# Kernel tuning notes

Hardware: AMD Instinct MI355X
Metric: run time of the kernel (lower is better)

The kernel has to match this reference:

```python
import jax, jax.numpy as jnp
import numpy as np


def _grid_mesh(n):
    ys, xs = np.meshgrid(np.arange(n), np.arange(n), indexing='ij')
    verts = np.stack([xs, ys, np.zeros_like(xs)], -1).reshape(-1, 3).astype(np.float32) / (n - 1)
    idx = np.arange(n * n).reshape(n, n)
    v00 = idx[:-1, :-1].ravel(); v01 = idx[:-1, 1:].ravel()
    v10 = idx[1:, :-1].ravel(); v11 = idx[1:, 1:].ravel()
    faces = np.concatenate([np.stack([v00, v10, v01], 1), np.stack([v01, v10, v11], 1)], 0).astype(np.int32)
    e = np.concatenate([faces[:, [0, 1]], faces[:, [1, 2]], faces[:, [2, 0]]], 0)
    e = np.unique(np.sort(e, axis=1), axis=0).astype(np.int32)
    return verts, faces, e


def setup_inputs() -> dict:
    N_GRID, B, S = 200, 2, 5000
    verts_np, faces_np, edges_np = _grid_mesh(N_GRID)
    verts_np[:, 2] = 0.1 * np.sin(2 * np.pi * verts_np[:, 0]) * np.sin(2 * np.pi * verts_np[:, 1])
    key = jax.random.key(0)
    k1, k2, k3, k4 = jax.random.split(key, 4)
    verts_std = jnp.asarray(verts_np)
    verts_scr = verts_std[None] + 5e-4 * jax.random.normal(k1, (B,) + verts_std.shape, jnp.float32)
    xy = jax.random.uniform(k2, (B, S, 2), jnp.float32)
    z = 0.1 * jnp.sin(2 * jnp.pi * xy[..., 0]) * jnp.sin(2 * jnp.pi * xy[..., 1])
    trg_points = jnp.concatenate([xy, z[..., None]], -1)
    rand_face_u = jax.random.uniform(k3, (B, S), jnp.float32)
    rand_bary = jax.random.uniform(k4, (B, S, 2), jnp.float32)
    return {
        'verts_scr': verts_scr,
        'verts_std': verts_std,
        'trg_points': trg_points,
        'rand_face_u': rand_face_u,
        'rand_bary': rand_bary,
        'faces': jnp.asarray(faces_np),
        'edges': jnp.asarray(edges_np),
    }


def _cot_edges(verts, faces):
    # pytorch3d cot_laplacian: per-face cotangents, symmetrized edge list (6F entries).
    v0, v1, v2 = verts[faces[:, 0]], verts[faces[:, 1]], verts[faces[:, 2]]
    A = jnp.linalg.norm(v1 - v2, axis=1)
    B = jnp.linalg.norm(v0 - v2, axis=1)
    C = jnp.linalg.norm(v0 - v1, axis=1)
    A2, B2, C2 = A * A, B * B, C * C
    s = 0.5 * (A + B + C)
    area = jnp.sqrt(jnp.clip(s * (s - A) * (s - B) * (s - C), 1e-12, None))
    cot = jnp.stack([B2 + C2 - A2, A2 + C2 - B2, A2 + B2 - C2], axis=1) / (4.0 * area[:, None])
    ii = faces[:, jnp.array([1, 2, 0])].reshape(-1)
    jj = faces[:, jnp.array([2, 0, 1])].reshape(-1)
    src = jnp.concatenate([ii, jj])
    dst = jnp.concatenate([jj, ii])
    w = jnp.concatenate([cot.reshape(-1), cot.reshape(-1)])
    return src, dst, w


def _sample_points(verts, faces, u_face, r_bary):
    # area-weighted face sampling + pytorch3d barycentric coords
    v0, v1, v2 = verts[faces[:, 0]], verts[faces[:, 1]], verts[faces[:, 2]]
    areas = 0.5 * jnp.linalg.norm(jnp.cross(v1 - v0, v2 - v0), axis=1)
    cdf = jnp.cumsum(areas) / jnp.sum(areas)
    fidx = jnp.clip(jnp.searchsorted(cdf, u_face), 0, faces.shape[0] - 1)
    su = jnp.sqrt(r_bary[:, 0])
    w0, w1, w2 = 1.0 - su, su * (1.0 - r_bary[:, 1]), su * r_bary[:, 1]
    return w0[:, None] * v0[fidx] + w1[:, None] * v1[fidx] + w2[:, None] * v2[fidx]


def _chamfer(x, y):
    # squared-distance chamfer, mean over points then batch (pytorch3d defaults)
    d = (jnp.sum(x * x, -1)[:, :, None] + jnp.sum(y * y, -1)[:, None, :]
         - 2.0 * jnp.einsum('bsd,btd->bst', x, y))
    return jnp.min(d, 2).mean() + jnp.min(d, 1).mean()


def _forward(verts_scr, verts_std, trg_points, rand_face_u, rand_bary, faces, edges):
    Vn = verts_std.shape[0]
    # chamfer between sampled src surface points and target point cloud
    sample_scr = jax.vmap(lambda v, u, r: _sample_points(v, faces, u, r))(verts_scr, rand_face_u, rand_bary)
    loss_p0 = _chamfer(sample_scr, trg_points)
    loss_n1 = jnp.asarray(1e-5, verts_scr.dtype)  # tensor-target branch

    # cot laplacian smoothing (method='cot')
    def lap_one(v):
        src, dst, w = _cot_edges(v, faces)
        Lv = jax.ops.segment_sum(w[:, None] * v[dst], src, num_segments=Vn)
        rw = jax.ops.segment_sum(w, src, num_segments=Vn)
        inv = jnp.where(rw > 0, 1.0 / jnp.maximum(rw, 1e-12), 0.0)
        return jnp.linalg.norm(Lv * inv[:, None] - v, axis=1).mean()

    loss_lap = jax.vmap(lap_one)(verts_scr).mean()

    # edge loss against mean edge length of the std mesh
    target_len = jnp.linalg.norm(verts_std[edges[:, 0]] - verts_std[edges[:, 1]], axis=1).mean()
    elen = jnp.linalg.norm(verts_scr[:, edges[:, 0]] - verts_scr[:, edges[:, 1]], axis=-1)
    loss_edge = ((elen - target_len) ** 2).mean()

    # ARAP rigid loss on std-mesh cot connectivity/weights
    src, dst, w = _cot_edges(verts_std, faces)
    e_std = verts_std[src] - verts_std[dst]

    def rigid_one(v):
        e_scr = v[src] - v[dst]
        S = jax.ops.segment_sum(w[:, None, None] * e_std[:, :, None] * e_scr[:, None, :], src, num_segments=Vn)
        U, _, Vt = jnp.linalg.svd(S)
        R = jnp.matmul(jnp.swapaxes(Vt, -1, -2), jnp.swapaxes(U, -1, -2))
        flip = jnp.where(jnp.linalg.det(R) < 0, -1.0, 1.0)
        Vt2 = Vt.at[:, -1, :].multiply(flip[:, None])
        R = jnp.matmul(jnp.swapaxes(Vt2, -1, -2), jnp.swapaxes(U, -1, -2))
        res = e_scr - jnp.einsum('eij,ej->ei', R[src], e_std)
        return jax.ops.segment_sum(w * jnp.sum(res * res, 1), src, num_segments=Vn)

    loss_rigid = jax.vmap(rigid_one)(verts_scr).mean()
    return jnp.stack([loss_p0, loss_n1, loss_lap, loss_edge, loss_rigid])


def reference(verts_scr, verts_std, trg_points, rand_face_u, rand_bary, faces, edges):
    return _forward(verts_scr, verts_std, trg_points, rand_face_u, rand_bary, faces, edges)
```

## Files before the change

kernel.cpp:

```cpp
#include <hip/hip_runtime.h>
#include <math.h>

#define TPB 256
#define MAXDEG 8

static __device__ __forceinline__ void atomAddD(double* p, double v) {
  __hip_atomic_fetch_add(p, v, __ATOMIC_RELAXED, __HIP_MEMORY_SCOPE_AGENT);
}

static __device__ __forceinline__ double bredsum(double v) {
  __shared__ double sb[TPB];
  int t = threadIdx.x;
  sb[t] = v;
  __syncthreads();
  for (int o = TPB / 2; o > 0; o >>= 1) {
    if (t < o) sb[t] += sb[t + o];
    __syncthreads();
  }
  double r = sb[0];
  __syncthreads();
  return r;
}

template <int p, int q, int r>
static __device__ __forceinline__ void jrot(double A[3][3], double V[3][3]) {
  double apq = A[p][q];
  if (apq == 0.0) return;
  double app = A[p][p], aqq = A[q][q];
  double theta = (aqq - app) / (2.0 * apq);
  double t = 1.0 / (fabs(theta) + sqrt(theta * theta + 1.0));
  if (theta < 0.0) t = -t;
  double c = 1.0 / sqrt(t * t + 1.0), sn = t * c;
  A[p][p] = app - t * apq;
  A[q][q] = aqq + t * apq;
  A[p][q] = 0.0;
  A[q][p] = 0.0;
  double arp = A[r][p], arq = A[r][q];
  A[r][p] = c * arp - sn * arq; A[p][r] = A[r][p];
  A[r][q] = sn * arp + c * arq; A[q][r] = A[r][q];
#pragma unroll
  for (int k = 0; k < 3; k++) {
    double vkp = V[k][p], vkq = V[k][q];
    V[k][p] = c * vkp - sn * vkq;
    V[k][q] = sn * vkp + c * vkq;
  }
}

#define ESWAP(la, lax, lay, laz, lb, lbx, lby, lbz)                       \
  if (la < lb) {                                                          \
    double t_;                                                            \
    t_ = la; la = lb; lb = t_;                                            \
    t_ = lax; lax = lbx; lbx = t_;                                        \
    t_ = lay; lay = lby; lby = t_;                                        \
    t_ = laz; laz = lbz; lbz = t_;                                        \
  }

static __device__ void kabschR(const double S[3][3], double R9[9]) {
  double A[3][3];
#pragma unroll
  for (int a = 0; a < 3; a++)
#pragma unroll
    for (int c = 0; c < 3; c++)
      A[a][c] = S[0][a] * S[0][c] + S[1][a] * S[1][c] + S[2][a] * S[2][c];
  double V[3][3] = {{1, 0, 0}, {0, 1, 0}, {0, 0, 1}};
  for (int sw = 0; sw < 12; sw++) {
    double off = fabs(A[0][1]) + fabs(A[0][2]) + fabs(A[1][2]);
    double dia = fabs(A[0][0]) + fabs(A[1][1]) + fabs(A[2][2]);
    if (!(off > dia * 1e-15)) break;
    jrot<0, 1, 2>(A, V);
    jrot<0, 2, 1>(A, V);
    jrot<1, 2, 0>(A, V);
  }
  double l0 = A[0][0], l1 = A[1][1], l2 = A[2][2];
  double a0x = V[0][0], a0y = V[1][0], a0z = V[2][0];
  double a1x = V[0][1], a1y = V[1][1], a1z = V[2][1];
  double a2x = V[0][2], a2y = V[1][2], a2z = V[2][2];
  ESWAP(l0, a0x, a0y, a0z, l1, a1x, a1y, a1z);
  ESWAP(l0, a0x, a0y, a0z, l2, a2x, a2y, a2z);
  ESWAP(l1, a1x, a1y, a1z, l2, a2x, a2y, a2z);
  double R00 = 1, R01 = 0, R02 = 0, R10 = 0, R11 = 1, R12 = 0, R20 = 0, R21 = 0, R22 = 1;
  double b1x = S[0][0] * a0x + S[0][1] * a0y + S[0][2] * a0z;
  double b1y = S[1][0] * a0x + S[1][1] * a0y + S[1][2] * a0z;
  double b1z = S[2][0] * a0x + S[2][1] * a0y + S[2][2] * a0z;
  double b2x = S[0][0] * a1x + S[0][1] * a1y + S[0][2] * a1z;
  double b2y = S[1][0] * a1x + S[1][1] * a1y + S[1][2] * a1z;
  double b2z = S[2][0] * a1x + S[2][1] * a1y + S[2][2] * a1z;
  double n1 = sqrt(b1x * b1x + b1y * b1y + b1z * b1z);
  if (n1 > 1e-300 && isfinite(n1)) {
    double u1x = b1x / n1, u1y = b1y / n1, u1z = b1z / n1;
    double dp = u1x * b2x + u1y * b2y + u1z * b2z;
    b2x -= dp * u1x; b2y -= dp * u1y; b2z -= dp * u1z;
    double n2 = sqrt(b2x * b2x + b2y * b2y + b2z * b2z);
    double u2x, u2y, u2z;
    if (n2 > n1 * 1e-14) {
      u2x = b2x / n2; u2y = b2y / n2; u2z = b2z / n2;
    } else {
      double f0 = fabs(u1x), f1 = fabs(u1y), f2 = fabs(u1z);
      double e0, e1, e2;
      if (f0 <= f1 && f0 <= f2) { e0 = 1.0 - u1x * u1x; e1 = -u1x * u1y; e2 = -u1x * u1z; }
      else if (f1 <= f2)        { e0 = -u1y * u1x; e1 = 1.0 - u1y * u1y; e2 = -u1y * u1z; }
      else                      { e0 = -u1z * u1x; e1 = -u1z * u1y; e2 = 1.0 - u1z * u1z; }
      double nw = sqrt(e0 * e0 + e1 * e1 + e2 * e2);
      u2x = e0 / nw; u2y = e1 / nw; u2z = e2 / nw;
    }
    double u3x = u1y * u2z - u1z * u2y;
    double u3y = u1z * u2x - u1x * u2z;
    double u3z = u1x * u2y - u1y * u2x;
    double w3x = a0y * a1z - a0z * a1y;
    double w3y = a0z * a1x - a0x * a1z;
    double w3z = a0x * a1y - a0y * a1x;
    R00 = a0x * u1x + a1x * u2x + w3x * u3x;
    R01 = a0x * u1y + a1x * u2y + w3x * u3y;
    R02 = a0x * u1z + a1x * u2z + w3x * u3z;
    R10 = a0y * u1x + a1y * u2x + w3y * u3x;
    R11 = a0y * u1y + a1y * u2y + w3y * u3y;
    R12 = a0y * u1z + a1y * u2z + w3y * u3z;
    R20 = a0z * u1x + a1z * u2x + w3z * u3x;
    R21 = a0z * u1y + a1z * u2y + w3z * u3y;
    R22 = a0z * u1z + a1z * u2z + w3z * u3z;
  }
  R9[0] = R00; R9[1] = R01; R9[2] = R02;
  R9[3] = R10; R9[4] = R11; R9[5] = R12;
  R9[6] = R20; R9[7] = R21; R9[8] = R22;
}

static __device__ __forceinline__ void heronCots(double A2, double B2, double C2,
                                                 double* c0, double* c1, double* c2) {
  double A = sqrt(A2), Bl = sqrt(B2), C = sqrt(C2);
  double s = 0.5 * (A + Bl + C);
  double pr = s * (s - A) * (s - Bl) * (s - C);
  pr = pr < 1e-12 ? 1e-12 : pr;
  double inv4 = 1.0 / (4.0 * sqrt(pr));
  *c0 = (B2 + C2 - A2) * inv4;
  *c1 = (A2 + C2 - B2) * inv4;
  *c2 = (A2 + B2 - C2) * inv4;
}

__global__ void kPrep(const float* vscr, const float* vstd, const int* faces,
                      const int* edges, double* cdf, double* ccot, double* scot,
                      int* adjcnt, int4* adjtab, double* accEdgeStd,
                      int B, int Vn, int F, int E) {
  int i = blockIdx.x * TPB + threadIdx.x;
  if (i < B * F) {
    int b = i / F, f = i % F;
    const float* vb = vscr + (size_t)b * Vn * 3;
    int i0 = faces[f * 3], i1 = faces[f * 3 + 1], i2 = faces[f * 3 + 2];
    {
      double p0x = vb[i0 * 3], p0y = vb[i0 * 3 + 1], p0z = vb[i0 * 3 + 2];
      double p1x = vb[i1 * 3], p1y = vb[i1 * 3 + 1], p1z = vb[i1 * 3 + 2];
      double p2x = vb[i2 * 3], p2y = vb[i2 * 3 + 1], p2z = vb[i2 * 3 + 2];
      double ax = p1x - p0x, ay = p1y - p0y, az = p1z - p0z;
      double bx = p2x - p0x, by = p2y - p0y, bz = p2z - p0z;
      double cx = ay * bz - az * by, cy = az * bx - ax * bz, cz = ax * by - ay * bx;
      cdf[i] = 0.5 * sqrt(cx * cx + cy * cy + cz * cz);
      double dx = p1x - p2x, dy = p1y - p2y, dz = p1z - p2z;
      double A2 = dx * dx + dy * dy + dz * dz;
      double B2 = bx * bx + by * by + bz * bz;
      double C2 = ax * ax + ay * ay + az * az;
      double c0, c1, c2;
      heronCots(A2, B2, C2, &c0, &c1, &c2);
      ccot[(size_t)i * 3 + 0] = c0;
      ccot[(size_t)i * 3 + 1] = c1;
      ccot[(size_t)i * 3 + 2] = c2;
    }
    if (b == 0) {
      double p0x = vstd[i0 * 3], p0y = vstd[i0 * 3 + 1], p0z = vstd[i0 * 3 + 2];
      double p1x = vstd[i1 * 3], p1y = vstd[i1 * 3 + 1], p1z = vstd[i1 * 3 + 2];
      double p2x = vstd[i2 * 3], p2y = vstd[i2 * 3 + 1], p2z = vstd[i2 * 3 + 2];
      double ax = p1x - p0x, ay = p1y - p0y, az = p1z - p0z;
      double bx = p2x - p0x, by = p2y - p0y, bz = p2z - p0z;
      double dx = p1x - p2x, dy = p1y - p2y, dz = p1z - p2z;
      double A2 = dx * dx + dy * dy + dz * dz;
      double B2 = bx * bx + by * by + bz * bz;
      double C2 = ax * ax + ay * ay + az * az;
      double c0, c1, c2;
      heronCots(A2, B2, C2, &c0, &c1, &c2);
      scot[(size_t)f * 3 + 0] = c0;
      scot[(size_t)f * 3 + 1] = c1;
      scot[(size_t)f * 3 + 2] = c2;
      int f3 = f * 3;
      int s0 = atomicAdd(&adjcnt[i0], 1);
      if (s0 < MAXDEG) adjtab[(size_t)i0 * MAXDEG + s0] = make_int4(i1, i2, f3 + 1, f3 + 2);
      int s1 = atomicAdd(&adjcnt[i1], 1);
      if (s1 < MAXDEG) adjtab[(size_t)i1 * MAXDEG + s1] = make_int4(i2, i0, f3 + 2, f3 + 0);
      int s2 = atomicAdd(&adjcnt[i2], 1);
      if (s2 < MAXDEG) adjtab[(size_t)i2 * MAXDEG + s2] = make_int4(i0, i1, f3 + 0, f3 + 1);
    }
  }
  double eval = 0.0;
  if (i < E) {
    int e0 = edges[(size_t)i * 2], e1 = edges[(size_t)i * 2 + 1];
    double dx = (double)vstd[e0 * 3 + 0] - vstd[e1 * 3 + 0];
    double dy = (double)vstd[e0 * 3 + 1] - vstd[e1 * 3 + 1];
    double dz = (double)vstd[e0 * 3 + 2] - vstd[e1 * 3 + 2];
    eval = sqrt(dx * dx + dy * dy + dz * dz);
  }
  double r = bredsum(eval);
  if (threadIdx.x == 0) atomAddD(accEdgeStd, r);
}

__global__ void kScanFused(double* a, double* bsum, double* boffs, int F, int nc,
                           int B, int* cnt) {
  int blk = blockIdx.x;
  int b = blk / nc, c = blk % nc;
  int t = threadIdx.x, lane = t & 63, wid = t >> 6;
  int f = c * 1024 + t;
  size_t idx = (size_t)b * F + f;
  double v = (f < F) ? a[idx] : 0.0;
  double x = v;
#pragma unroll
  for (int o = 1; o < 64; o <<= 1) {
    double y = __shfl_up(x, o, 64);
    if (lane >= o) x += y;
  }
  __shared__ double wsum[16];
  __shared__ double woffs[16];
  if (lane == 63) wsum[wid] = x;
  __syncthreads();
  if (wid == 0) {
    double s = (lane < 16) ? wsum[lane] : 0.0;
    double xs = s;
#pragma unroll
    for (int o = 1; o < 16; o <<= 1) {
      double y = __shfl_up(xs, o, 64);
      if (lane >= o) xs += y;
    }
    double ex = __shfl_up(xs, 1, 64);
    if (lane < 16) woffs[lane] = (lane == 0) ? 0.0 : ex;
  }
  __syncthreads();
  x += woffs[wid];
  if (f < F) a[idx] = x;
  if (t == 1023) bsum[(size_t)b * nc + c] = x;
  __syncthreads();
  __shared__ int amlast;
  if (t == 0) {
    __threadfence();
    int old = __hip_atomic_fetch_add(cnt, 1, __ATOMIC_ACQ_REL, __HIP_MEMORY_SCOPE_AGENT);
    amlast = (old == (int)gridDim.x - 1) ? 1 : 0;
  }
  __syncthreads();
  if (amlast && wid == 0) {
    for (int bb = 0; bb < B; bb++) {
      double carry = 0.0;
      for (int base = 0; base < nc; base += 64) {
        int cc = base + lane;
        double s = (cc < nc) ? bsum[(size_t)bb * nc + cc] : 0.0;
        double xs = s;
#pragma unroll
        for (int o = 1; o < 64; o <<= 1) {
          double y = __shfl_up(xs, o, 64);
          if (lane >= o) xs += y;
        }
        double ex = __shfl_up(xs, 1, 64);
        double excl = (lane == 0) ? 0.0 : ex;
        if (cc < nc) boffs[(size_t)bb * nc + cc] = carry + excl;
        carry += __shfl(xs, 63, 64);
      }
    }
  }
}

__global__ void kSample(const float* verts, const int* faces, const double* cdf,
                        const double* bsum, const double* boffs,
                        const float* rfu, const float* rbary, float* samples,
                        int B, int Vn, int F, int S, int nc) {
  int i = blockIdx.x * blockDim.x + threadIdx.x;
  if (i >= B * S) return;
  int b = i / S;
  const double* bo = boffs + (size_t)b * nc;
  const double* bs = bsum + (size_t)b * nc;
  double total = bo[nc - 1] + bs[nc - 1];
  double tgt = (double)rfu[i] * total;
  int lo = 0, hi = nc;
  while (lo < hi) {
    int m = (lo + hi) >> 1;
    if (bo[m] + bs[m] < tgt) lo = m + 1; else hi = m;
  }
  int c = lo < nc ? lo : nc - 1;
  double thr = tgt - bo[c];
  const double* cc = cdf + (size_t)b * F + (size_t)c * 1024;
  int lim = F - c * 1024; if (lim > 1024) lim = 1024;
  lo = 0; hi = lim;
  while (lo < hi) {
    int m = (lo + hi) >> 1;
    if (cc[m] < thr) lo = m + 1; else hi = m;
  }
  int j = lo < lim ? lo : lim - 1;
  int f = c * 1024 + j;
  const float* vb = verts + (size_t)b * Vn * 3;
  int i0 = faces[f * 3], i1 = faces[f * 3 + 1], i2 = faces[f * 3 + 2];
  float r0 = rbary[(size_t)i * 2], r1 = rbary[(size_t)i * 2 + 1];
  float su = sqrtf(r0);
  float w0 = 1.f - su, w1 = su * (1.f - r1), w2 = su * r1;
  samples[(size_t)i * 3 + 0] = w0 * vb[i0 * 3 + 0] + w1 * vb[i1 * 3 + 0] + w2 * vb[i2 * 3 + 0];
  samples[(size_t)i * 3 + 1] = w0 * vb[i0 * 3 + 1] + w1 * vb[i1 * 3 + 1] + w2 * vb[i2 * 3 + 1];
  samples[(size_t)i * 3 + 2] = w0 * vb[i0 * 3 + 2] + w1 * vb[i1 * 3 + 2] + w2 * vb[i2 * 3 + 2];
}

__global__ void kChamferBoth(const float* smp, const float* trg, unsigned* rowmin,
                             int B, int S) {
  int z = blockIdx.z;
  int dir = z / B, b = z % B;
  const float* X = dir ? trg : smp;
  const float* Y = dir ? smp : trg;
  int i = blockIdx.x * TPB + threadIdx.x;
  int j0 = blockIdx.y * TPB;
  int n = min(TPB, S - j0);
  __shared__ float4 sy[TPB];
  const float* Yb = Y + ((size_t)b * S + j0) * 3;
  if ((int)threadIdx.x < n) {
    int t = threadIdx.x;
    sy[t] = make_float4(Yb[t * 3], Yb[t * 3 + 1], Yb[t * 3 + 2], 0.f);
  }
  __syncthreads();
  if (i >= S) return;
  const float* Xb = X + (size_t)b * S * 3;
  float x0 = Xb[i * 3], x1 = Xb[i * 3 + 1], x2 = Xb[i * 3 + 2];
  float inf = __int_as_float(0x7f800000);
  float m0 = inf, m1 = inf, m2 = inf, m3 = inf;
  int k = 0;
  for (; k + 4 <= n; k += 4) {
    float4 y0 = sy[k], y1 = sy[k + 1], y2 = sy[k + 2], y3 = sy[k + 3];
    float a0 = x0 - y0.x, b0 = x1 - y0.y, c0 = x2 - y0.z;
    float a1 = x0 - y1.x, b1 = x1 - y1.y, c1 = x2 - y1.z;
    float a2 = x0 - y2.x, b2 = x1 - y2.y, c2 = x2 - y2.z;
    float a3 = x0 - y3.x, b3 = x1 - y3.y, c3 = x2 - y3.z;
    m0 = fminf(m0, a0 * a0 + b0 * b0 + c0 * c0);
    m1 = fminf(m1, a1 * a1 + b1 * b1 + c1 * c1);
    m2 = fminf(m2, a2 * a2 + b2 * b2 + c2 * c2);
    m3 = fminf(m3, a3 * a3 + b3 * b3 + c3 * c3);
  }
  for (; k < n; k++) {
    float4 y = sy[k];
    float a = x0 - y.x, bb = x1 - y.y, cc = x2 - y.z;
    m0 = fminf(m0, a * a + bb * bb + cc * cc);
  }
  float mn = fminf(fminf(m0, m1), fminf(m2, m3));
  atomicMin(&rowmin[((size_t)dir * B + b) * S + i], __float_as_uint(mn));
}

__global__ void kMisc(const unsigned* rm, int nrm, const float* vscr, const int* edges,
                      int B, int Vn, int E, const double* tacc,
                      double* accCh, double* accEd) {
  int i = blockIdx.x * TPB + threadIdx.x;
  double v = 0.0;
  if (i < nrm) v = (double)__uint_as_float(rm[i]);
  double r = bredsum(v);
  if (threadIdx.x == 0) atomAddD(accCh, r);
  double tl = tacc[0] / (double)E;
  double val = 0.0;
  if (i < B * E) {
    int b = i / E, e = i % E;
    const float* vb = vscr + (size_t)b * Vn * 3;
    int e0 = edges[(size_t)e * 2], e1 = edges[(size_t)e * 2 + 1];
    double dx = (double)vb[e0 * 3 + 0] - vb[e1 * 3 + 0];
    double dy = (double)vb[e0 * 3 + 1] - vb[e1 * 3 + 1];
    double dz = (double)vb[e0 * 3 + 2] - vb[e1 * 3 + 2];
    double l = sqrt(dx * dx + dy * dy + dz * dz);
    double d = l - tl;
    val = d * d;
  }
  double r2 = bredsum(val);
  if (threadIdx.x == 0) atomAddD(accEd, r2);
}

__global__ void kVertexFin(const float* vstd, const float* vscr,
                           const int* cnt, const int4* adjtab, const double* scot,
                           const double* ccot, int B, int Vn, int F,
                           double* accum, int* done, float* out, int S, int E) {
  int idx = blockIdx.x * TPB + threadIdx.x;
  double vlap = 0.0, vrig = 0.0;
  if (idx < B * Vn) {
    int b = idx / Vn, v = idx % Vn;
    const float* cb = vscr + (size_t)b * Vn * 3;
    const double* ccb = ccot + (size_t)b * F * 3;
    double pasx = vstd[v * 3], pasy = vstd[v * 3 + 1], pasz = vstd[v * 3 + 2];
    double pacx = cb[v * 3], pacy = cb[v * 3 + 1], pacz = cb[v * 3 + 2];
    int n = cnt[v];
    if (n > MAXDEG) n = MAXDEG;
    const int4* at = adjtab + (size_t)v * MAXDEG;
    double S00 = 0, S01 = 0, S02 = 0, S10 = 0, S11 = 0, S12 = 0, S20 = 0, S21 = 0, S22 = 0;
    double Lx = 0, Ly = 0, Lz = 0, rw = 0, Qs = 0, Qc = 0;
    for (int k = 0; k < n; k++) {
      int4 e = at[k];
      int jb = e.x, jc = e.y;
      double cBs = scot[e.z], cCs = scot[e.w];
      double cBc = ccb[e.z], cCc = ccb[e.w];
      double pbsx = vstd[jb * 3], pbsy = vstd[jb * 3 + 1], pbsz = vstd[jb * 3 + 2];
      double pcsx = vstd[jc * 3], pcsy = vstd[jc * 3 + 1], pcsz = vstd[jc * 3 + 2];
      double pbcx = cb[jb * 3], pbcy = cb[jb * 3 + 1], pbcz = cb[jb * 3 + 2];
      double pccx = cb[jc * 3], pccy = cb[jc * 3 + 1], pccz = cb[jc * 3 + 2];
      Lx += cCc * pbcx + cBc * pccx;
      Ly += cCc * pbcy + cBc * pccy;
      Lz += cCc * pbcz + cBc * pccz;
      rw += cBc + cCc;
      double e1sx = pasx - pbsx, e1sy = pasy - pbsy, e1sz = pasz - pbsz;
      double e2sx = pasx - pcsx, e2sy = pasy - pcsy, e2sz = pasz - pcsz;
      double e1cx = pacx - pbcx, e1cy = pacy - pbcy, e1cz = pacz - pbcz;
      double e2cx = pacx - pccx, e2cy = pacy - pccy, e2cz = pacz - pccz;
      S00 += cCs * e1sx * e1cx + cBs * e2sx * e2cx;
      S01 += cCs * e1sx * e1cy + cBs * e2sx * e2cy;
      S02 += cCs * e1sx * e1cz + cBs * e2sx * e2cz;
      S10 += cCs * e1sy * e1cx + cBs * e2sy * e2cx;
      S11 += cCs * e1sy * e1cy + cBs * e2sy * e2cy;
      S12 += cCs * e1sy * e1cz + cBs * e2sy * e2cz;
      S20 += cCs * e1sz * e1cx + cBs * e2sz * e2cx;
      S21 += cCs * e1sz * e1cy + cBs * e2sz * e2cy;
      S22 += cCs * e1sz * e1cz + cBs * e2sz * e2cz;
      Qs += cCs * (e1sx * e1sx + e1sy * e1sy + e1sz * e1sz)
          + cBs * (e2sx * e2sx + e2sy * e2sy + e2sz * e2sz);
      Qc += cCs * (e1cx * e1cx + e1cy * e1cy + e1cz * e1cz)
          + cBs * (e2cx * e2cx + e2cy * e2cy + e2cz * e2cz);
    }
    double inv = (rw > 0.0) ? 1.0 / fmax(rw, 1e-12) : 0.0;
    double dx = Lx * inv - pacx, dy = Ly * inv - pacy, dz = Lz * inv - pacz;
    vlap = sqrt(dx * dx + dy * dy + dz * dz);
    double S[3][3] = {{S00, S01, S02}, {S10, S11, S12}, {S20, S21, S22}};
    double R9[9];
    kabschR(S, R9);
    double trRS = R9[0] * S00 + R9[1] * S10 + R9[2] * S20
                + R9[3] * S01 + R9[4] * S11 + R9[5] * S21
                + R9[6] * S02 + R9[7] * S12 + R9[8] * S22;
    vrig = Qc + Qs - 2.0 * trRS;
  }
  double r1 = bredsum(vlap);
  if (threadIdx.x == 0) atomAddD(accum + 1, r1);
  double r2 = bredsum(vrig);
  if (threadIdx.x == 0) atomAddD(accum + 4, r2);
  __shared__ int amlast;
  if (threadIdx.x == 0) {
    __threadfence();
    int old = __hip_atomic_fetch_add(done, 1, __ATOMIC_ACQ_REL, __HIP_MEMORY_SCOPE_AGENT);
    amlast = (old == (int)gridDim.x - 1) ? 1 : 0;
  }
  __syncthreads();
  if (amlast && threadIdx.x == 0) {
    double a0 = __hip_atomic_load(accum + 0, __ATOMIC_RELAXED, __HIP_MEMORY_SCOPE_AGENT);
    double a1 = __hip_atomic_load(accum + 1, __ATOMIC_RELAXED, __HIP_MEMORY_SCOPE_AGENT);
    double a3 = __hip_atomic_load(accum + 3, __ATOMIC_RELAXED, __HIP_MEMORY_SCOPE_AGENT);
    double a4 = __hip_atomic_load(accum + 4, __ATOMIC_RELAXED, __HIP_MEMORY_SCOPE_AGENT);
    out[0] = (float)(a0 / ((double)B * S));
    out[1] = 1e-5f;
    out[2] = (float)(a1 / ((double)B * Vn));
    out[3] = (float)(a3 / ((double)B * E));
    out[4] = (float)(a4 / ((double)B * Vn));
  }
}

extern "C" void kernel_launch(void* const* d_in, const int* in_sizes, int n_in,
                              void* d_out, int out_size, void* d_ws, size_t ws_size,
                              hipStream_t stream) {
  const float* vscr = (const float*)d_in[0];
  const float* vstd = (const float*)d_in[1];
  const float* trg  = (const float*)d_in[2];
  const float* rfu  = (const float*)d_in[3];
  const float* rby  = (const float*)d_in[4];
  const int* faces  = (const int*)d_in[5];
  const int* edges  = (const int*)d_in[6];
  float* out = (float*)d_out;

  int nVs = in_sizes[1];
  int Vn = nVs / 3;
  int B = in_sizes[0] / nVs;
  int S = in_sizes[3] / B;
  int F = in_sizes[5] / 3;
  int E = in_sizes[6] / 2;
  int nc = (F + 1023) / 1024;

  char* p = (char*)d_ws;
  auto alloc = [&](size_t bytes) -> void* {
    void* r = (void*)p;
    p += (bytes + 255) & ~(size_t)255;
    return r;
  };
  double* cdf   = (double*)alloc((size_t)B * F * sizeof(double));
  double* bsum  = (double*)alloc((size_t)B * nc * sizeof(double));
  double* boffs = (double*)alloc((size_t)B * nc * sizeof(double));
  double* scot  = (double*)alloc((size_t)F * 3 * sizeof(double));
  double* ccot  = (double*)alloc((size_t)B * F * 3 * sizeof(double));
  float* samples   = (float*)alloc((size_t)B * S * 3 * sizeof(float));
  unsigned* rowmin = (unsigned*)alloc((size_t)2 * B * S * sizeof(unsigned));
  int4* adjtab  = (int4*)alloc((size_t)Vn * MAXDEG * sizeof(int4));
  size_t zbytes = (size_t)Vn * sizeof(int) + 8 * sizeof(int) + 8 * sizeof(double);
  char* zbase   = (char*)alloc(zbytes);
  int* adjcnt   = (int*)zbase;
  int* cnts     = (int*)(zbase + (size_t)Vn * sizeof(int));
  double* accum = (double*)(zbase + (size_t)Vn * sizeof(int) + 8 * sizeof(int));

  hipMemsetAsync(zbase, 0, zbytes, stream);
  int nrm = 2 * B * S;
  hipMemsetAsync(rowmin, 0xFF, (size_t)nrm * sizeof(unsigned), stream);

  int BF = B * F;
  kPrep<<<(BF + TPB - 1) / TPB, TPB, 0, stream>>>(vscr, vstd, faces, edges, cdf, ccot,
                                                  scot, adjcnt, adjtab, accum + 2,
                                                  B, Vn, F, E);
  kScanFused<<<B * nc, 1024, 0, stream>>>(cdf, bsum, boffs, F, nc, B, cnts + 0);
  kSample<<<(B * S + TPB - 1) / TPB, TPB, 0, stream>>>(vscr, faces, cdf, bsum, boffs,
                                                       rfu, rby, samples, B, Vn, F, S, nc);
  dim3 cg((S + TPB - 1) / TPB, (S + TPB - 1) / TPB, 2 * B);
  kChamferBoth<<<cg, TPB, 0, stream>>>(samples, trg, rowmin, B, S);
  int nmisc = nrm > B * E ? nrm : B * E;
  kMisc<<<(nmisc + TPB - 1) / TPB, TPB, 0, stream>>>(rowmin, nrm, vscr, edges, B, Vn, E,
                                                     accum + 2, accum + 0, accum + 3);
  kVertexFin<<<(B * Vn + TPB - 1) / TPB, TPB, 0, stream>>>(vstd, vscr, adjcnt, adjtab,
                                                           scot, ccot, B, Vn, F,
                                                           accum, cnts + 1, out, S, E);
}
```

Measured before the change: 197.4 us.

## Fuse vertex ARAP/Laplacian work with chamfer blocks, fold rowmin init into prep

Merges the per-vertex Laplacian/ARAP kernel and the chamfer nearest-neighbour kernel into one launch: the leading blocks handle vertices and the remaining blocks handle chamfer tiles, so the two independent workloads run concurrently. The misc reduction and the final output write are merged into one last kernel. The rowmin memset moves into kPrep, and the Jacobi sweep cap drops from 12 to 8. Together these remove two launches and a memset and let the double-precision vertex work overlap the FP32 chamfer work. The risks are an inactive branch holding registers and shared memory in every block, and slightly less converged eigenvectors.

```diff
diff --git a/kernel.cpp b/kernel.cpp
--- a/kernel.cpp
+++ b/kernel.cpp
@@ -63,7 +63,7 @@
     for (int c = 0; c < 3; c++)
       A[a][c] = S[0][a] * S[0][c] + S[1][a] * S[1][c] + S[2][a] * S[2][c];
   double V[3][3] = {{1, 0, 0}, {0, 1, 0}, {0, 0, 1}};
-  for (int sw = 0; sw < 12; sw++) {
+  for (int sw = 0; sw < 8; sw++) {
     double off = fabs(A[0][1]) + fabs(A[0][2]) + fabs(A[1][2]);
     double dia = fabs(A[0][0]) + fabs(A[1][1]) + fabs(A[2][2]);
     if (!(off > dia * 1e-15)) break;
@@ -139,8 +139,9 @@
 __global__ void kPrep(const float* vscr, const float* vstd, const int* faces,
                       const int* edges, double* cdf, double* ccot, double* scot,
                       int* adjcnt, int4* adjtab, double* accEdgeStd,
-                      int B, int Vn, int F, int E) {
+                      unsigned* rowmin, int nrm, int B, int Vn, int F, int E) {
   int i = blockIdx.x * TPB + threadIdx.x;
+  if (i < nrm) rowmin[i] = 0xFFFFFFFFu;
   if (i < B * F) {
     int b = i / F, f = i % F;
     const float* vb = vscr + (size_t)b * Vn * 3;
@@ -298,57 +299,125 @@
   samples[(size_t)i * 3 + 2] = w0 * vb[i0 * 3 + 2] + w1 * vb[i1 * 3 + 2] + w2 * vb[i2 * 3 + 2];
 }
 
-__global__ void kChamferBoth(const float* smp, const float* trg, unsigned* rowmin,
-                             int B, int S) {
-  int z = blockIdx.z;
-  int dir = z / B, b = z % B;
-  const float* X = dir ? trg : smp;
-  const float* Y = dir ? smp : trg;
-  int i = blockIdx.x * TPB + threadIdx.x;
-  int j0 = blockIdx.y * TPB;
-  int n = min(TPB, S - j0);
-  __shared__ float4 sy[TPB];
-  const float* Yb = Y + ((size_t)b * S + j0) * 3;
-  if ((int)threadIdx.x < n) {
-    int t = threadIdx.x;
-    sy[t] = make_float4(Yb[t * 3], Yb[t * 3 + 1], Yb[t * 3 + 2], 0.f);
-  }
-  __syncthreads();
-  if (i >= S) return;
-  const float* Xb = X + (size_t)b * S * 3;
-  float x0 = Xb[i * 3], x1 = Xb[i * 3 + 1], x2 = Xb[i * 3 + 2];
-  float inf = __int_as_float(0x7f800000);
-  float m0 = inf, m1 = inf, m2 = inf, m3 = inf;
-  int k = 0;
-  for (; k + 4 <= n; k += 4) {
-    float4 y0 = sy[k], y1 = sy[k + 1], y2 = sy[k + 2], y3 = sy[k + 3];
-    float a0 = x0 - y0.x, b0 = x1 - y0.y, c0 = x2 - y0.z;
-    float a1 = x0 - y1.x, b1 = x1 - y1.y, c1 = x2 - y1.z;
-    float a2 = x0 - y2.x, b2 = x1 - y2.y, c2 = x2 - y2.z;
-    float a3 = x0 - y3.x, b3 = x1 - y3.y, c3 = x2 - y3.z;
-    m0 = fminf(m0, a0 * a0 + b0 * b0 + c0 * c0);
-    m1 = fminf(m1, a1 * a1 + b1 * b1 + c1 * c1);
-    m2 = fminf(m2, a2 * a2 + b2 * b2 + c2 * c2);
-    m3 = fminf(m3, a3 * a3 + b3 * b3 + c3 * c3);
-  }
-  for (; k < n; k++) {
-    float4 y = sy[k];
-    float a = x0 - y.x, bb = x1 - y.y, cc = x2 - y.z;
-    m0 = fminf(m0, a * a + bb * bb + cc * cc);
-  }
-  float mn = fminf(fminf(m0, m1), fminf(m2, m3));
-  atomicMin(&rowmin[((size_t)dir * B + b) * S + i], __float_as_uint(mn));
-}
-
-__global__ void kMisc(const unsigned* rm, int nrm, const float* vscr, const int* edges,
-                      int B, int Vn, int E, const double* tacc,
-                      double* accCh, double* accEd) {
+__global__ void kFat(const float* vstd, const float* vscr,
+                     const int* cnt, const int4* adjtab, const double* scot,
+                     const double* ccot, const float* smp, const float* trg,
+                     unsigned* rowmin, int nv, int ncx, int B, int Vn, int F, int S,
+                     double* accum) {
+  if ((int)blockIdx.x < nv) {
+    int idx = blockIdx.x * TPB + threadIdx.x;
+    double vlap = 0.0, vrig = 0.0;
+    if (idx < B * Vn) {
+      int b = idx / Vn, v = idx % Vn;
+      const float* cb = vscr + (size_t)b * Vn * 3;
+      const double* ccb = ccot + (size_t)b * F * 3;
+      double pasx = vstd[v * 3], pasy = vstd[v * 3 + 1], pasz = vstd[v * 3 + 2];
+      double pacx = cb[v * 3], pacy = cb[v * 3 + 1], pacz = cb[v * 3 + 2];
+      int n = cnt[v];
+      if (n > MAXDEG) n = MAXDEG;
+      const int4* at = adjtab + (size_t)v * MAXDEG;
+      double S00 = 0, S01 = 0, S02 = 0, S10 = 0, S11 = 0, S12 = 0, S20 = 0, S21 = 0, S22 = 0;
+      double Lx = 0, Ly = 0, Lz = 0, rw = 0, Qs = 0, Qc = 0;
+      for (int k = 0; k < n; k++) {
+        int4 e = at[k];
+        int jb = e.x, jc = e.y;
+        double cBs = scot[e.z], cCs = scot[e.w];
+        double cBc = ccb[e.z], cCc = ccb[e.w];
+        double pbsx = vstd[jb * 3], pbsy = vstd[jb * 3 + 1], pbsz = vstd[jb * 3 + 2];
+        double pcsx = vstd[jc * 3], pcsy = vstd[jc * 3 + 1], pcsz = vstd[jc * 3 + 2];
+        double pbcx = cb[jb * 3], pbcy = cb[jb * 3 + 1], pbcz = cb[jb * 3 + 2];
+        double pccx = cb[jc * 3], pccy = cb[jc * 3 + 1], pccz = cb[jc * 3 + 2];
+        Lx += cCc * pbcx + cBc * pccx;
+        Ly += cCc * pbcy + cBc * pccy;
+        Lz += cCc * pbcz + cBc * pccz;
+        rw += cBc + cCc;
+        double e1sx = pasx - pbsx, e1sy = pasy - pbsy, e1sz = pasz - pbsz;
+        double e2sx = pasx - pcsx, e2sy = pasy - pcsy, e2sz = pasz - pcsz;
+        double e1cx = pacx - pbcx, e1cy = pacy - pbcy, e1cz = pacz - pbcz;
+        double e2cx = pacx - pccx, e2cy = pacy - pccy, e2cz = pacz - pccz;
+        S00 += cCs * e1sx * e1cx + cBs * e2sx * e2cx;
+        S01 += cCs * e1sx * e1cy + cBs * e2sx * e2cy;
+        S02 += cCs * e1sx * e1cz + cBs * e2sx * e2cz;
+        S10 += cCs * e1sy * e1cx + cBs * e2sy * e2cx;
+        S11 += cCs * e1sy * e1cy + cBs * e2sy * e2cy;
+        S12 += cCs * e1sy * e1cz + cBs * e2sy * e2cz;
+        S20 += cCs * e1sz * e1cx + cBs * e2sz * e2cx;
+        S21 += cCs * e1sz * e1cy + cBs * e2sz * e2cy;
+        S22 += cCs * e1sz * e1cz + cBs * e2sz * e2cz;
+        Qs += cCs * (e1sx * e1sx + e1sy * e1sy + e1sz * e1sz)
+            + cBs * (e2sx * e2sx + e2sy * e2sy + e2sz * e2sz);
+        Qc += cCs * (e1cx * e1cx + e1cy * e1cy + e1cz * e1cz)
+            + cBs * (e2cx * e2cx + e2cy * e2cy + e2cz * e2cz);
+      }
+      double inv = (rw > 0.0) ? 1.0 / fmax(rw, 1e-12) : 0.0;
+      double dx = Lx * inv - pacx, dy = Ly * inv - pacy, dz = Lz * inv - pacz;
+      vlap = sqrt(dx * dx + dy * dy + dz * dz);
+      double Smat[3][3] = {{S00, S01, S02}, {S10, S11, S12}, {S20, S21, S22}};
+      double R9[9];
+      kabschR(Smat, R9);
+      double trRS = R9[0] * S00 + R9[1] * S10 + R9[2] * S20
+                  + R9[3] * S01 + R9[4] * S11 + R9[5] * S21
+                  + R9[6] * S02 + R9[7] * S12 + R9[8] * S22;
+      vrig = Qc + Qs - 2.0 * trRS;
+    }
+    double r1 = bredsum(vlap);
+    if (threadIdx.x == 0) atomAddD(accum + 1, r1);
+    double r2 = bredsum(vrig);
+    if (threadIdx.x == 0) atomAddD(accum + 4, r2);
+  } else {
+    int cid = blockIdx.x - nv;
+    int bx = cid % ncx;
+    int by = (cid / ncx) % ncx;
+    int z = cid / (ncx * ncx);
+    int dir = z / B, b = z % B;
+    const float* X = dir ? trg : smp;
+    const float* Y = dir ? smp : trg;
+    int i = bx * TPB + threadIdx.x;
+    int j0 = by * TPB;
+    int n = min(TPB, S - j0);
+    __shared__ float4 sy[TPB];
+    const float* Yb = Y + ((size_t)b * S + j0) * 3;
+    if ((int)threadIdx.x < n) {
+      int t = threadIdx.x;
+      sy[t] = make_float4(Yb[t * 3], Yb[t * 3 + 1], Yb[t * 3 + 2], 0.f);
+    }
+    __syncthreads();
+    if (i >= S) return;
+    const float* Xb = X + (size_t)b * S * 3;
+    float x0 = Xb[i * 3], x1 = Xb[i * 3 + 1], x2 = Xb[i * 3 + 2];
+    float inf = __int_as_float(0x7f800000);
+    float m0 = inf, m1 = inf, m2 = inf, m3 = inf;
+    int k = 0;
+    for (; k + 4 <= n; k += 4) {
+      float4 y0 = sy[k], y1 = sy[k + 1], y2 = sy[k + 2], y3 = sy[k + 3];
+      float a0 = x0 - y0.x, b0 = x1 - y0.y, c0 = x2 - y0.z;
+      float a1 = x0 - y1.x, b1 = x1 - y1.y, c1 = x2 - y1.z;
+      float a2 = x0 - y2.x, b2 = x1 - y2.y, c2 = x2 - y2.z;
+      float a3 = x0 - y3.x, b3 = x1 - y3.y, c3 = x2 - y3.z;
+      m0 = fminf(m0, a0 * a0 + b0 * b0 + c0 * c0);
+      m1 = fminf(m1, a1 * a1 + b1 * b1 + c1 * c1);
+      m2 = fminf(m2, a2 * a2 + b2 * b2 + c2 * c2);
+      m3 = fminf(m3, a3 * a3 + b3 * b3 + c3 * c3);
+    }
+    for (; k < n; k++) {
+      float4 y = sy[k];
+      float a = x0 - y.x, bb = x1 - y.y, cc = x2 - y.z;
+      m0 = fminf(m0, a * a + bb * bb + cc * cc);
+    }
+    float mn = fminf(fminf(m0, m1), fminf(m2, m3));
+    atomicMin(&rowmin[((size_t)dir * B + b) * S + i], __float_as_uint(mn));
+  }
+}
+
+__global__ void kMiscFin(const unsigned* rm, int nrm, const float* vscr,
+                         const int* edges, int B, int Vn, int E,
+                         double* accum, int* done, float* out, int S) {
   int i = blockIdx.x * TPB + threadIdx.x;
   double v = 0.0;
   if (i < nrm) v = (double)__uint_as_float(rm[i]);
   double r = bredsum(v);
-  if (threadIdx.x == 0) atomAddD(accCh, r);
-  double tl = tacc[0] / (double)E;
+  if (threadIdx.x == 0) atomAddD(accum + 0, r);
+  double tl = accum[2] / (double)E;
   double val = 0.0;
   if (i < B * E) {
     int b = i / E, e = i % E;
@@ -362,72 +431,7 @@
     val = d * d;
   }
   double r2 = bredsum(val);
-  if (threadIdx.x == 0) atomAddD(accEd, r2);
-}
-
-__global__ void kVertexFin(const float* vstd, const float* vscr,
-                           const int* cnt, const int4* adjtab, const double* scot,
-                           const double* ccot, int B, int Vn, int F,
-                           double* accum, int* done, float* out, int S, int E) {
-  int idx = blockIdx.x * TPB + threadIdx.x;
-  double vlap = 0.0, vrig = 0.0;
-  if (idx < B * Vn) {
-    int b = idx / Vn, v = idx % Vn;
-    const float* cb = vscr + (size_t)b * Vn * 3;
-    const double* ccb = ccot + (size_t)b * F * 3;
-    double pasx = vstd[v * 3], pasy = vstd[v * 3 + 1], pasz = vstd[v * 3 + 2];
-    double pacx = cb[v * 3], pacy = cb[v * 3 + 1], pacz = cb[v * 3 + 2];
-    int n = cnt[v];
-    if (n > MAXDEG) n = MAXDEG;
-    const int4* at = adjtab + (size_t)v * MAXDEG;
-    double S00 = 0, S01 = 0, S02 = 0, S10 = 0, S11 = 0, S12 = 0, S20 = 0, S21 = 0, S22 = 0;
-    double Lx = 0, Ly = 0, Lz = 0, rw = 0, Qs = 0, Qc = 0;
-    for (int k = 0; k < n; k++) {
-      int4 e = at[k];
-      int jb = e.x, jc = e.y;
-      double cBs = scot[e.z], cCs = scot[e.w];
-      double cBc = ccb[e.z], cCc = ccb[e.w];
-      double pbsx = vstd[jb * 3], pbsy = vstd[jb * 3 + 1], pbsz = vstd[jb * 3 + 2];
-      double pcsx = vstd[jc * 3], pcsy = vstd[jc * 3 + 1], pcsz = vstd[jc * 3 + 2];
-      double pbcx = cb[jb * 3], pbcy = cb[jb * 3 + 1], pbcz = cb[jb * 3 + 2];
-      double pccx = cb[jc * 3], pccy = cb[jc * 3 + 1], pccz = cb[jc * 3 + 2];
-      Lx += cCc * pbcx + cBc * pccx;
-      Ly += cCc * pbcy + cBc * pccy;
-      Lz += cCc * pbcz + cBc * pccz;
-      rw += cBc + cCc;
-      double e1sx = pasx - pbsx, e1sy = pasy - pbsy, e1sz = pasz - pbsz;
-      double e2sx = pasx - pcsx, e2sy = pasy - pcsy, e2sz = pasz - pcsz;
-      double e1cx = pacx - pbcx, e1cy = pacy - pbcy, e1cz = pacz - pbcz;
-      double e2cx = pacx - pccx, e2cy = pacy - pccy, e2cz = pacz - pccz;
-      S00 += cCs * e1sx * e1cx + cBs * e2sx * e2cx;
-      S01 += cCs * e1sx * e1cy + cBs * e2sx * e2cy;
-      S02 += cCs * e1sx * e1cz + cBs * e2sx * e2cz;
-      S10 += cCs * e1sy * e1cx + cBs * e2sy * e2cx;
-      S11 += cCs * e1sy * e1cy + cBs * e2sy * e2cy;
-      S12 += cCs * e1sy * e1cz + cBs * e2sy * e2cz;
-      S20 += cCs * e1sz * e1cx + cBs * e2sz * e2cx;
-      S21 += cCs * e1sz * e1cy + cBs * e2sz * e2cy;
-      S22 += cCs * e1sz * e1cz + cBs * e2sz * e2cz;
-      Qs += cCs * (e1sx * e1sx + e1sy * e1sy + e1sz * e1sz)
-          + cBs * (e2sx * e2sx + e2sy * e2sy + e2sz * e2sz);
-      Qc += cCs * (e1cx * e1cx + e1cy * e1cy + e1cz * e1cz)
-          + cBs * (e2cx * e2cx + e2cy * e2cy + e2cz * e2cz);
-    }
-    double inv = (rw > 0.0) ? 1.0 / fmax(rw, 1e-12) : 0.0;
-    double dx = Lx * inv - pacx, dy = Ly * inv - pacy, dz = Lz * inv - pacz;
-    vlap = sqrt(dx * dx + dy * dy + dz * dz);
-    double S[3][3] = {{S00, S01, S02}, {S10, S11, S12}, {S20, S21, S22}};
-    double R9[9];
-    kabschR(S, R9);
-    double trRS = R9[0] * S00 + R9[1] * S10 + R9[2] * S20
-                + R9[3] * S01 + R9[4] * S11 + R9[5] * S21
-                + R9[6] * S02 + R9[7] * S12 + R9[8] * S22;
-    vrig = Qc + Qs - 2.0 * trRS;
-  }
-  double r1 = bredsum(vlap);
-  if (threadIdx.x == 0) atomAddD(accum + 1, r1);
-  double r2 = bredsum(vrig);
-  if (threadIdx.x == 0) atomAddD(accum + 4, r2);
+  if (threadIdx.x == 0) atomAddD(accum + 3, r2);
   __shared__ int amlast;
   if (threadIdx.x == 0) {
     __threadfence();
@@ -490,21 +494,22 @@
 
   hipMemsetAsync(zbase, 0, zbytes, stream);
   int nrm = 2 * B * S;
-  hipMemsetAsync(rowmin, 0xFF, (size_t)nrm * sizeof(unsigned), stream);
 
   int BF = B * F;
   kPrep<<<(BF + TPB - 1) / TPB, TPB, 0, stream>>>(vscr, vstd, faces, edges, cdf, ccot,
                                                   scot, adjcnt, adjtab, accum + 2,
-                                                  B, Vn, F, E);
+                                                  rowmin, nrm, B, Vn, F, E);
   kScanFused<<<B * nc, 1024, 0, stream>>>(cdf, bsum, boffs, F, nc, B, cnts + 0);
   kSample<<<(B * S + TPB - 1) / TPB, TPB, 0, stream>>>(vscr, faces, cdf, bsum, boffs,
                                                        rfu, rby, samples, B, Vn, F, S, nc);
-  dim3 cg((S + TPB - 1) / TPB, (S + TPB - 1) / TPB, 2 * B);
-  kChamferBoth<<<cg, TPB, 0, stream>>>(samples, trg, rowmin, B, S);
+  int nv = (B * Vn + TPB - 1) / TPB;
+  int ncx = (S + TPB - 1) / TPB;
+  int nch = ncx * ncx * 2 * B;
+  kFat<<<nv + nch, TPB, 0, stream>>>(vstd, vscr, adjcnt, adjtab, scot, ccot,
+                                     samples, trg, rowmin, nv, ncx, B, Vn, F, S,
+                                     accum);
   int nmisc = nrm > B * E ? nrm : B * E;
-  kMisc<<<(nmisc + TPB - 1) / TPB, TPB, 0, stream>>>(rowmin, nrm, vscr, edges, B, Vn, E,
-                                                     accum + 2, accum + 0, accum + 3);
-  kVertexFin<<<(B * Vn + TPB - 1) / TPB, TPB, 0, stream>>>(vstd, vscr, adjcnt, adjtab,
-                                                           scot, ccot, B, Vn, F,
-                                                           accum, cnts + 1, out, S, E);
-}
+  kMiscFin<<<(nmisc + TPB - 1) / TPB, TPB, 0, stream>>>(rowmin, nrm, vscr, edges,
+                                                        B, Vn, E, accum, cnts + 1,
+                                                        out, S);
+}
```

New measurement: 208.2 us. +5.5%, slower.
